# Performance work log

Hardware: AMD Instinct MI355X
Metric: run time of the kernel (lower is better)

The kernel has to match this reference:

```python
import jax, jax.numpy as jnp
import numpy as np

B, LD = 256, 64
NO, LO = 10240, 32
NM, LM = 81920, 16
EO, EM = 81920, 327680
E, HID, H, Dh, V = 128, 256, 8, 16, 10000


def masked_mean(tokens, table):
    # tokens: [N, L] int; pad id = 0
    emb = table[tokens]                            # [N, L, E]
    mask = (tokens != 0)
    s = jnp.sum(emb * mask[..., None].astype(emb.dtype), axis=1)
    lens = jnp.maximum(jnp.sum(mask, axis=1), 1).astype(emb.dtype)
    return s / lens[:, None]


def segment_softmax(scores, seg, num_segments):
    # scores: [E, ...]; softmax over entries sharing seg id (PyG softmax)
    m = jax.ops.segment_max(scores, seg, num_segments=num_segments)
    e = jnp.exp(scores - m[seg])
    s = jax.ops.segment_sum(e, seg, num_segments=num_segments)
    return e / (s[seg] + 1e-16)


def gcn_conv(x, W, b, src, dst, n):
    # PyG GCNConv: normalize=True, add_self_loops=True
    xw = x @ W
    loops = jnp.arange(n, dtype=src.dtype)
    s2 = jnp.concatenate([src, loops])
    d2 = jnp.concatenate([dst, loops])
    deg = jax.ops.segment_sum(jnp.ones_like(d2, dtype=x.dtype), d2, num_segments=n)
    dinv = deg ** -0.5  # deg >= 1 due to self loops
    norm = dinv[s2] * dinv[d2]
    out = jax.ops.segment_sum(xw[s2] * norm[:, None], d2, num_segments=n)
    return out + b


def transformer_conv(x, Wq, bq, Wk, bk, Wv, bv, Wskip, bskip, src, dst, n):
    q = (x @ Wq + bq).reshape(n, H, Dh)
    k = (x @ Wk + bk).reshape(n, H, Dh)
    v = (x @ Wv + bv).reshape(n, H, Dh)
    score = jnp.sum(q[dst] * k[src], axis=-1) / jnp.sqrt(jnp.asarray(Dh, x.dtype))  # [E, H]
    alpha = segment_softmax(score, dst, n)
    agg = jax.ops.segment_sum(alpha[:, :, None] * v[src], dst, num_segments=n)  # [n, H, Dh]
    return agg.reshape(n, H * Dh) + x @ Wskip + bskip


def global_attention(x, Wg, bg, seg, num_segments):
    gate = x @ Wg + bg                              # [N, 1]
    a = segment_softmax(gate, seg, num_segments)
    return jax.ops.segment_sum(a * x, seg, num_segments=num_segments)


def setup_inputs():
    key = jax.random.key(0)
    ks = jax.random.split(key, 20)
    sc = lambda k, shape: jax.random.normal(k, shape, dtype=jnp.float32) * 0.05
    inp = {
        "desc_tokens": jax.random.randint(ks[0], (B, LD), 0, V, dtype=jnp.int32),
        "x_tokens": jax.random.randint(ks[1], (NO, LO), 0, V, dtype=jnp.int32),
        "mini_tokens": jax.random.randint(ks[2], (NM, LM), 0, V, dtype=jnp.int32),
        "src": jax.random.randint(ks[3], (EO,), 0, NO, dtype=jnp.int32),
        "dst": jax.random.randint(ks[4], (EO,), 0, NO, dtype=jnp.int32),
        "mini_src": jax.random.randint(ks[5], (EM,), 0, NM, dtype=jnp.int32),
        "mini_dst": jax.random.randint(ks[6], (EM,), 0, NM, dtype=jnp.int32),
        "mini_batch": (jnp.arange(NM, dtype=jnp.int32) // (NM // NO)),
        "node_batch": (jnp.arange(NO, dtype=jnp.int32) // (NO // B)),
        "desc_table": sc(ks[7], (V, E)),
        "code_table": sc(ks[8], (V, E)),
        "code_table2": sc(ks[9], (V, E)),
        "Wq": sc(ks[10], (E, H * Dh)), "bq": jnp.zeros((H * Dh,), jnp.float32),
        "Wk": sc(ks[11], (E, H * Dh)), "bk": jnp.zeros((H * Dh,), jnp.float32),
        "Wv": sc(ks[12], (E, H * Dh)), "bv": jnp.zeros((H * Dh,), jnp.float32),
        "Wskip": sc(ks[13], (E, H * Dh)), "bskip": jnp.zeros((H * Dh,), jnp.float32),
        "W2": sc(ks[14], (E, HID)), "b2": jnp.zeros((HID,), jnp.float32),
        "W3": sc(ks[15], (HID, E)), "b3": jnp.zeros((E,), jnp.float32),
        "Wg": sc(ks[16], (E, 1)), "bg": jnp.zeros((1,), jnp.float32),
    }
    return inp


def reference(desc_tokens, x_tokens, mini_tokens, src, dst, mini_src, mini_dst,
              mini_batch, node_batch, desc_table, code_table, code_table2,
              Wq, bq, Wk, bk, Wv, bv, Wskip, bskip, W2, b2, W3, b3, Wg, bg):
    # encode_desc: embedding + masked mean pool -> [B, E]
    h_n = masked_mean(desc_tokens, desc_table)
    # encode_code_graph
    stmt_emb = masked_mean(x_tokens, code_table2)          # [NO, E]
    mini_emb = masked_mean(mini_tokens, code_table)        # [NM, E]
    mini_hidden = transformer_conv(mini_emb, Wq, bq, Wk, bk, Wv, bv,
                                   Wskip, bskip, mini_src, mini_dst, NM)
    mini_fn = global_attention(mini_hidden, Wg, bg, mini_batch, NO)  # [NO, E]
    mini_fn = (mini_fn + stmt_emb) * 0.5
    h = jax.nn.relu(gcn_conv(mini_fn, W2, b2, src, dst, NO))
    final_stmt = gcn_conv(h, W3, b3, src, dst, NO)
    fn_repr = global_attention(final_stmt, Wg, bg, node_batch, B)    # [B, E]
    # cosine similarity (torch eps=1e-8 clamps each norm)
    na = jnp.maximum(jnp.linalg.norm(fn_repr, axis=-1), 1e-8)
    nb = jnp.maximum(jnp.linalg.norm(h_n, axis=-1), 1e-8)
    return jnp.sum(fn_repr * h_n, axis=-1) / (na * nb)
```

## Files before the change

### kernel.cpp

```cpp
#include <hip/hip_runtime.h>
#include <hip/hip_bf16.h>
#include <math.h>

#define BB   256
#define LDE  64
#define NO   10240
#define LO   32
#define NM   81920
#define LM   16
#define EO   81920
#define EM   327680
#define ED   128
#define HIDD 256
#define NH   8
#define DH   16
#define VV   10000

static inline int nblk(long long n, int b) { return (int)((n + b - 1) / b); }

typedef __attribute__((ext_vector_type(8))) short short8;
typedef __attribute__((ext_vector_type(4))) float f32x4;

static __device__ __forceinline__ unsigned short bf16_rne(float f) {
  unsigned u = __float_as_uint(f);
  return (unsigned short)((u + 0x7fffu + ((u >> 16) & 1u)) >> 16);
}
static __device__ __forceinline__ float bf16_to_f(unsigned short h) {
  return __uint_as_float(((unsigned)h) << 16);
}
static __device__ __forceinline__ float4 b4f(ushort4 h) {
  return make_float4(bf16_to_f(h.x), bf16_to_f(h.y), bf16_to_f(h.z), bf16_to_f(h.w));
}
static __device__ __forceinline__ ushort4 f4b(float4 v) {
  return make_ushort4(bf16_rne(v.x), bf16_rne(v.y), bf16_rne(v.z), bf16_rne(v.w));
}

static __device__ __forceinline__ void gl_lds16(const void* g, void* l) {
  __builtin_amdgcn_global_load_lds(
      (const __attribute__((address_space(1))) unsigned int*)g,
      (__attribute__((address_space(3))) unsigned int*)l, 16, 0, 0);
}

struct ConvArgs {
  const float *Wq, *Wk, *Wv, *Ws, *W2, *W3;
  const float *bq, *bk, *bv, *bs;
  short8* frag;
  float* bias512;
  const float* t1; unsigned short* o1;
  const float* t2; unsigned short* o2;
  int* hist;
};
#define TBLK (2 * VV * ED / 4 / 256)
#define ZBLK ((NM + NO) / 256)
__global__ void __launch_bounds__(256)
conv_all_k(ConvArgs A) {
  int b = blockIdx.x;
  if (b < 32) {
    int g = b * 256 + threadIdx.x;
    int lane = g & 63, f = g >> 6;
    int jl = f & 7, kb = (f >> 3) & 3, ch = f >> 5;
    int cf = ch * 8 + jl;
    int c = cf * 16 + (lane & 15);
    int k0 = kb * 32 + ((lane >> 4) << 3);
    const float* wp; int cm;
    if (c < 128)      { wp = A.Wq; cm = c; }
    else if (c < 384) { int u = c - 128, t = u & 7;
                        wp = (t < 4) ? A.Wk : A.Wv; cm = (u >> 3) * 4 + (t & 3); }
    else              { wp = A.Ws; cm = c - 384; }
    short8 h;
    #pragma unroll
    for (int j = 0; j < 8; ++j)
      h[j] = (short)bf16_rne(wp[(size_t)(k0 + j) * 128 + cm]);
    A.frag[g] = h;
  } else if (b < 64) {
    int g = (b - 32) * 256 + threadIdx.x;
    const float* wp; int M, dstbase, gg;
    if (g < 4096) { wp = A.W2; M = 256; dstbase = 8192;  gg = g; }
    else          { wp = A.W3; M = 128; dstbase = 12288; gg = g - 4096; }
    int lane = gg & 63, fid = gg >> 6;
    int nt = fid % (M / 16), kb = fid / (M / 16);
    int n = nt * 16 + (lane & 15);
    int k0 = kb * 32 + ((lane >> 4) << 3);
    short8 h;
    #pragma unroll
    for (int j = 0; j < 8; ++j)
      h[j] = (short)bf16_rne(wp[(size_t)(k0 + j) * M + n]);
    A.frag[dstbase + gg] = h;
  } else if (b < 64 + TBLK) {
    int q = (b - 64) * 256 + threadIdx.x;
    const int NT = VV * ED / 4;
    if (q < NT) {
      float4 v = *(const float4*)(A.t1 + (size_t)q * 4);
      *(ushort4*)(A.o1 + (size_t)q * 4) = f4b(v);
    } else if (q < 2 * NT) {
      int q2 = q - NT;
      float4 v = *(const float4*)(A.t2 + (size_t)q2 * 4);
      *(ushort4*)(A.o2 + (size_t)q2 * 4) = f4b(v);
    }
  } else if (b < 64 + TBLK + ZBLK) {
    int i = (b - 64 - TBLK) * 256 + threadIdx.x;
    if (i < NM + NO) A.hist[i] = 0;
  } else {
    for (int c = threadIdx.x; c < 512; c += 256) {
      float v;
      if (c < 128)      v = A.bq[c];
      else if (c < 384) { int u = c - 128, t = u & 7;
                          v = (t < 4) ? A.bk[(u >> 3) * 4 + t] : A.bv[(u >> 3) * 4 + (t & 3)]; }
      else              v = A.bs[c - 384];
      A.bias512[c] = v;
    }
  }
}

template<int L>
static __device__ __forceinline__ void embed_body_f(const int* __restrict__ tokens,
                                                    const float* __restrict__ table,
                                                    float* __restrict__ out, int blk) {
  const int r = threadIdx.x >> 5, lane = threadIdx.x & 31;
  const int n0 = blk * 8;
  __shared__ int toks[8][L];
  for (int i = threadIdx.x; i < 8 * L; i += 256)
    toks[i / L][i % L] = tokens[(size_t)n0 * L + i];
  __syncthreads();
  float4 acc = make_float4(0.f, 0.f, 0.f, 0.f);
  int cnt = 0;
  #pragma unroll
  for (int l = 0; l < L; ++l) {
    int t = toks[r][l];
    float4 v = *(const float4*)(table + (size_t)t * ED + lane * 4);
    float msk = (t != 0) ? 1.f : 0.f;
    cnt += (t != 0);
    acc.x = fmaf(msk, v.x, acc.x); acc.y = fmaf(msk, v.y, acc.y);
    acc.z = fmaf(msk, v.z, acc.z); acc.w = fmaf(msk, v.w, acc.w);
  }
  float inv = 1.f / (float)(cnt > 0 ? cnt : 1);
  acc.x *= inv; acc.y *= inv; acc.z *= inv; acc.w *= inv;
  *(float4*)(out + (size_t)(n0 + r) * ED + lane * 4) = acc;
}

template<int L>
static __device__ __forceinline__ void embed_body16b(const int* __restrict__ tokens,
                                                     const unsigned short* __restrict__ table,
                                                     unsigned short* __restrict__ out, int blk) {
  const int r = threadIdx.x >> 4, lane = threadIdx.x & 15;
  const int n0 = blk * 16;
  __shared__ int toks[16][L];
  for (int i = threadIdx.x; i < 16 * L; i += 256)
    toks[i / L][i % L] = tokens[(size_t)n0 * L + i];
  __syncthreads();
  float acc[8] = {};
  int cnt = 0;
  #pragma unroll
  for (int b0 = 0; b0 < L; b0 += 16) {
    short8 vv[16];
    #pragma unroll
    for (int l = 0; l < 16; ++l) {
      int t = toks[r][b0 + l];
      vv[l] = *(const short8*)(table + (size_t)t * ED + lane * 8);
    }
    #pragma unroll
    for (int l = 0; l < 16; ++l) {
      int t = toks[r][b0 + l];
      float msk = (t != 0) ? 1.f : 0.f;
      cnt += (t != 0);
      #pragma unroll
      for (int j = 0; j < 8; ++j)
        acc[j] = fmaf(msk, bf16_to_f((unsigned short)vv[l][j]), acc[j]);
    }
  }
  float inv = 1.f / (float)(cnt > 0 ? cnt : 1);
  short8 o;
  #pragma unroll
  for (int j = 0; j < 8; ++j) o[j] = (short)bf16_rne(acc[j] * inv);
  *(short8*)(out + (size_t)(n0 + r) * ED + lane * 8) = o;
}

#define HBLK ((EM + EO) / 256)
#define MBLK (NM / 16)
#define XBLK (NO / 16)
__global__ void __launch_bounds__(256)
embed_all_k(const int* __restrict__ desc_tokens, const float* __restrict__ desc_table,
            float* __restrict__ h_n,
            const int* __restrict__ x_tokens, const unsigned short* __restrict__ ctab2,
            unsigned short* __restrict__ stmt,
            const int* __restrict__ mini_tokens, const unsigned short* __restrict__ ctab,
            unsigned short* __restrict__ miniE,
            const int* __restrict__ mini_dst, const int* __restrict__ dst,
            int* __restrict__ histm, int* __restrict__ histo) {
  int b = blockIdx.x;
  if (b < MBLK) embed_body16b<LM>(mini_tokens, ctab, miniE, b);
  else if (b < MBLK + XBLK) embed_body16b<LO>(x_tokens, ctab2, stmt, b - MBLK);
  else if (b < MBLK + XBLK + BB / 8)
    embed_body_f<LDE>(desc_tokens, desc_table, h_n, b - MBLK - XBLK);
  else {
    int e = (b - MBLK - XBLK - BB / 8) * 256 + threadIdx.x;
    if (e < EM) atomicAdd(&histm[mini_dst[e]], 1);
    else        atomicAdd(&histo[dst[e - EM]], 1);
  }
}

__global__ void scan_partials2_k(int* __restrict__ p) {
  __shared__ int sd[512];
  int base = (blockIdx.x == 0) ? 0 : NM / 256;
  int B    = (blockIdx.x == 0) ? NM / 256 : NO / 256;
  int t = threadIdx.x;
  int v = (t < B) ? p[base + t] : 0;
  sd[t] = v; __syncthreads();
  for (int off = 1; off < 512; off <<= 1) {
    int a = (t >= off) ? sd[t - off] : 0;
    __syncthreads();
    sd[t] += a;
    __syncthreads();
  }
  if (t < B) p[base + t] = sd[t] - v;
}
__global__ void scan_final2_k(const int* __restrict__ hist, const int* __restrict__ partials,
                              int* __restrict__ offsm, int* __restrict__ curm,
                              int* __restrict__ offso, int* __restrict__ curo,
                              float* __restrict__ dinv) {
  __shared__ int sd[256];
  int i = blockIdx.x * 256 + threadIdx.x;
  int v = hist[i];
  sd[threadIdx.x] = v; __syncthreads();
  for (int off = 1; off < 256; off <<= 1) {
    int a = (threadIdx.x >= off) ? sd[threadIdx.x - off] : 0;
    __syncthreads();
    sd[threadIdx.x] += a;
    __syncthreads();
  }
  int excl = sd[threadIdx.x] - v + partials[blockIdx.x];
  if (i < NM) {
    offsm[i] = excl; curm[i] = excl;
    if (i == NM - 1) offsm[NM] = excl + v;
  } else {
    int i2 = i - NM;
    offso[i2] = excl; curo[i2] = excl;
    if (i2 == NO - 1) offso[NO] = excl + v;
    dinv[i2] = 1.f / sqrtf(1.f + (float)v);
  }
}
__global__ void scatter2_k(const int* __restrict__ sm, const int* __restrict__ dm,
                           int* __restrict__ cm, int* __restrict__ km,
                           const int* __restrict__ so, const int* __restrict__ dd,
                           int* __restrict__ co, int* __restrict__ ko) {
  int e = blockIdx.x * 256 + threadIdx.x;
  if (e < EM) {
    int pos = atomicAdd(&cm[dm[e]], 1);
    km[pos] = sm[e];
  } else {
    int e2 = e - EM;
    if (e2 < EO) {
      int pos = atomicAdd(&co[dd[e2]], 1);
      ko[pos] = so[e2];
    }
  }
}

#define QKVSB (NM / 128)
#define CSUMB ((NM + NO) / 256)
__global__ void __launch_bounds__(512)
qkvs_merged_k(const unsigned short* __restrict__ Ab, const short8* __restrict__ Wf,
              const float* __restrict__ bias512, unsigned short* __restrict__ out,
              const int* __restrict__ hist, int* __restrict__ part) {
  __shared__ short8 wlds[2048];
  const int tid = threadIdx.x;
  if (blockIdx.x >= QKVSB) {
    int* sd = (int*)wlds;
    const int cb = blockIdx.x - QKVSB;
    const int i = cb * 256 + (tid & 255);
    if (tid < 256) sd[tid] = (i < NM + NO) ? hist[i] : 0;
    __syncthreads();
    for (int s = 128; s > 0; s >>= 1) {
      if (tid < s) sd[tid] += sd[tid + s];
      __syncthreads();
    }
    if (tid == 0) part[cb] = sd[0];
    return;
  }
  const int id = blockIdx.x;
  const int blk = (id & 7) * 80 + (id >> 3);
  const int n0 = blk * 128;
  const int w = tid >> 6, lane = tid & 63;
  const int r = lane & 15, qd = lane >> 4;
  const int node = n0 + w * 16 + r;
  char* myl = (char*)wlds + w * 4096;

  short8 a[4];
  #pragma unroll
  for (int kb = 0; kb < 4; ++kb)
    a[kb] = *(const short8*)(Ab + (size_t)node * ED + kb * 32 + qd * 8);

  for (int ch = 0; ch < 4; ++ch) {
    {
      const char* gs = (const char*)Wf + (size_t)ch * 32768
                     + (size_t)(w * 4) * 1024 + (size_t)lane * 16;
      char* ls = (char*)wlds + (w * 4) * 1024;
      #pragma unroll
      for (int t = 0; t < 4; ++t)
        gl_lds16(gs + t * 1024, ls + t * 1024);
    }
    __syncthreads();

    f32x4 acc[8];
    #pragma unroll
    for (int jl = 0; jl < 8; ++jl) acc[jl] = (f32x4){0.f, 0.f, 0.f, 0.f};
    #pragma unroll
    for (int kb = 0; kb < 4; ++kb)
      #pragma unroll
      for (int jl = 0; jl < 8; ++jl) {
        short8 wf = *(const short8*)((const char*)wlds
                      + ((size_t)((kb << 3) | jl) * 64 + lane) * 16);
        acc[jl] = __builtin_amdgcn_mfma_f32_16x16x32_bf16(wf, a[kb], acc[jl], 0, 0, 0);
      }
    __syncthreads();

    #pragma unroll
    for (int jl = 0; jl < 8; ++jl) {
      const int cf = ch * 8 + jl;
      const float4 bv = *(const float4*)(bias512 + cf * 16 + qd * 4);
      ushort4 o;
      o.x = bf16_rne(acc[jl][0] + bv.x);
      o.y = bf16_rne(acc[jl][1] + bv.y);
      o.z = bf16_rne(acc[jl][2] + bv.z);
      o.w = bf16_rne(acc[jl][3] + bv.w);
      *(ushort4*)(myl + r * 256 + ((jl * 32) ^ ((r & 7) << 5)) + qd * 8) = o;
    }
    #pragma unroll
    for (int t = 0; t < 4; ++t) {
      const int rr = t * 4 + qd;
      short8 v = *(const short8*)(myl + rr * 256 + (((lane & 15) * 16) ^ ((rr & 7) << 5)));
      *(short8*)(out + (size_t)(n0 + w * 16 + rr) * 512 + ch * 128 + (lane & 15) * 8) = v;
    }
    __syncthreads();
  }
}

template<bool RELU>
__global__ void __launch_bounds__(512)
mgemm_b_k(const unsigned short* __restrict__ Ab, const short8* __restrict__ Bh,
          const float* __restrict__ bias, unsigned short* __restrict__ C,
          int K, int M) {
  const int bn0 = blockIdx.x * 128;
  const int n0 = blockIdx.y * 128;
  const int tid = threadIdx.x;
  const int w = tid >> 6, lane = tid & 63;
  const int wm = (w & 3) * 2, wn = (w >> 2) * 4;
  const int r = lane & 15, qd = lane >> 4;
  const int NTm = M / 16;
  f32x4 acc[2][4];
  #pragma unroll
  for (int i = 0; i < 2; ++i)
    #pragma unroll
    for (int j = 0; j < 4; ++j) acc[i][j] = (f32x4){0.f, 0.f, 0.f, 0.f};
  const int kbn = K / 32;
  for (int kb = 0; kb < kbn; ++kb) {
    short8 bh[4];
    #pragma unroll
    for (int j = 0; j < 4; ++j)
      bh[j] = Bh[((size_t)kb * NTm + (bn0 >> 4) + wn + j) * 64 + lane];
    short8 a[2];
    #pragma unroll
    for (int i = 0; i < 2; ++i)
      a[i] = *(const short8*)(Ab + (size_t)(n0 + (wm + i) * 16 + r) * K + kb * 32 + qd * 8);
    #pragma unroll
    for (int i = 0; i < 2; ++i)
      #pragma unroll
      for (int j = 0; j < 4; ++j)
        acc[i][j] = __builtin_amdgcn_mfma_f32_16x16x32_bf16(bh[j], a[i], acc[i][j], 0, 0, 0);
  }
  #pragma unroll
  for (int i = 0; i < 2; ++i)
    #pragma unroll
    for (int j = 0; j < 4; ++j) {
      const int node = n0 + (wm + i) * 16 + r;
      const int colb = bn0 + (wn + j) * 16 + qd * 4;
      float4 bv = bias ? *(const float4*)(bias + colb) : make_float4(0.f, 0.f, 0.f, 0.f);
      float v0 = acc[i][j][0] + bv.x;
      float v1 = acc[i][j][1] + bv.y;
      float v2 = acc[i][j][2] + bv.z;
      float v3 = acc[i][j][3] + bv.w;
      if (RELU) {
        v0 = fmaxf(v0, 0.f); v1 = fmaxf(v1, 0.f);
        v2 = fmaxf(v2, 0.f); v3 = fmaxf(v3, 0.f);
      }
      ushort4 o = make_ushort4(bf16_rne(v0), bf16_rne(v1), bf16_rne(v2), bf16_rne(v3));
      *(ushort4*)(C + (size_t)node * M + colb) = o;
    }
}

__global__ void __launch_bounds__(128)
attn_fused_k(unsigned short* buf,
             const int* __restrict__ offs, const int* __restrict__ csr,
             const float* __restrict__ Wg, const float* __restrict__ bg,
             float* __restrict__ gateOut) {
  const int g = threadIdx.x >> 5, lane = threadIdx.x & 31;
  const int n = blockIdx.x * 4 + g;
  float4 q = b4f(*(const ushort4*)(buf + (size_t)n * 512 + lane * 4));
  float4 sk = b4f(*(const ushort4*)(buf + (size_t)n * 512 + 384 + lane * 4));
  float4 wg = *(const float4*)(Wg + lane * 4);
  int lo = offs[n], hi = offs[n + 1];
  float4 O = make_float4(0.f, 0.f, 0.f, 0.f);
  float m = -INFINITY, l = 0.f;
  for (int base = lo; base < hi; base += 4) {
    int rem = hi - base;
    int sidx[4];
    #pragma unroll
    for (int i = 0; i < 4; ++i) sidx[i] = (i < rem) ? csr[base + i] : 0;
    short8 kvr[4];
    #pragma unroll
    for (int i = 0; i < 4; ++i)
      kvr[i] = *(const short8*)(buf + (size_t)sidx[i] * 512 + 128 + lane * 8);
    float sc[4]; float4 vt[4];
    #pragma unroll
    for (int i = 0; i < 4; ++i) {
      float4 kt = make_float4(bf16_to_f((unsigned short)kvr[i][0]),
                              bf16_to_f((unsigned short)kvr[i][1]),
                              bf16_to_f((unsigned short)kvr[i][2]),
                              bf16_to_f((unsigned short)kvr[i][3]));
      vt[i] = make_float4(bf16_to_f((unsigned short)kvr[i][4]),
                          bf16_to_f((unsigned short)kvr[i][5]),
                          bf16_to_f((unsigned short)kvr[i][6]),
                          bf16_to_f((unsigned short)kvr[i][7]));
      float p = q.x * kt.x + q.y * kt.y + q.z * kt.z + q.w * kt.w;
      p += __shfl_xor(p, 1, 64);
      p += __shfl_xor(p, 2, 64);
      sc[i] = (i < rem) ? p * 0.25f : -INFINITY;
    }
    float mt = fmaxf(fmaxf(sc[0], sc[1]), fmaxf(sc[2], sc[3]));
    float mn = fmaxf(m, mt);
    float scale = __expf(m - mn);
    float pe[4];
    #pragma unroll
    for (int i = 0; i < 4; ++i) pe[i] = __expf(sc[i] - mn);
    l = l * scale + ((pe[0] + pe[1]) + (pe[2] + pe[3]));
    O.x = fmaf(pe[3], vt[3].x, fmaf(pe[2], vt[2].x, fmaf(pe[1], vt[1].x, fmaf(pe[0], vt[0].x, O.x * scale))));
    O.y = fmaf(pe[3], vt[3].y, fmaf(pe[2], vt[2].y, fmaf(pe[1], vt[1].y, fmaf(pe[0], vt[0].y, O.y * scale))));
    O.z = fmaf(pe[3], vt[3].z, fmaf(pe[2], vt[2].z, fmaf(pe[1], vt[1].z, fmaf(pe[0], vt[0].z, O.z * scale))));
    O.w = fmaf(pe[3], vt[3].w, fmaf(pe[2], vt[2].w, fmaf(pe[1], vt[1].w, fmaf(pe[0], vt[0].w, O.w * scale))));
    m = mn;
  }
  float inv = 1.f / (l + 1e-16f);
  float4 out = make_float4(O.x * inv + sk.x, O.y * inv + sk.y,
                           O.z * inv + sk.z, O.w * inv + sk.w);
  *(ushort4*)(buf + (size_t)n * 512 + lane * 4) = f4b(out);
  float ps = out.x * wg.x + out.y * wg.y + out.z * wg.z + out.w * wg.w;
  #pragma unroll
  for (int o = 1; o <= 16; o <<= 1) ps += __shfl_xor(ps, o, 64);
  if (lane == 0) gateOut[n] = ps + bg[0];
}

__global__ void __launch_bounds__(256)
gcn_gather_b_k(const unsigned short* __restrict__ x, const float* __restrict__ dinv,
               const int* __restrict__ offs, const int* __restrict__ csr,
               const float* __restrict__ bias, unsigned short* __restrict__ out,
               const float* __restrict__ Wg, const float* __restrict__ bg,
               float* __restrict__ gateOut) {
  const int wv = threadIdx.x >> 6, lane = threadIdx.x & 63;
  const int half = lane >> 5, cl = lane & 31;
  const int n = blockIdx.x * 4 + wv;
  float di = dinv[n];
  float4 acc = make_float4(0.f, 0.f, 0.f, 0.f);
  if (half == 0) {
    float4 xs = b4f(*(const ushort4*)(x + (size_t)n * ED + cl * 4));
    float w0 = di * di;
    acc = make_float4(w0 * xs.x, w0 * xs.y, w0 * xs.z, w0 * xs.w);
  }
  int lo = offs[n], hi = offs[n + 1];
  for (int base = lo; base < hi; base += 8) {
    int sidx[4]; bool ok[4];
    #pragma unroll
    for (int i = 0; i < 4; ++i) {
      int e = base + 2 * i + half;
      ok[i] = e < hi;
      sidx[i] = ok[i] ? csr[e] : 0;
    }
    float dw[4];
    #pragma unroll
    for (int i = 0; i < 4; ++i) dw[i] = ok[i] ? di * dinv[sidx[i]] : 0.f;
    ushort4 vr[4];
    #pragma unroll
    for (int i = 0; i < 4; ++i)
      vr[i] = *(const ushort4*)(x + (size_t)sidx[i] * ED + cl * 4);
    #pragma unroll
    for (int i = 0; i < 4; ++i) {
      float4 v = b4f(vr[i]);
      acc.x = fmaf(dw[i], v.x, acc.x); acc.y = fmaf(dw[i], v.y, acc.y);
      acc.z = fmaf(dw[i], v.z, acc.z); acc.w = fmaf(dw[i], v.w, acc.w);
    }
  }
  acc.x += __shfl_xor(acc.x, 32, 64); acc.y += __shfl_xor(acc.y, 32, 64);
  acc.z += __shfl_xor(acc.z, 32, 64); acc.w += __shfl_xor(acc.w, 32, 64);
  if (bias) {
    float4 b4 = *(const float4*)(bias + cl * 4);
    acc.x += b4.x; acc.y += b4.y; acc.z += b4.z; acc.w += b4.w;
  }
  if (half == 0)
    *(ushort4*)(out + (size_t)n * ED + cl * 4) = f4b(acc);
  if (gateOut) {
    float4 wg = *(const float4*)(Wg + cl * 4);
    float ps = acc.x * wg.x + acc.y * wg.y + acc.z * wg.z + acc.w * wg.w;
    #pragma unroll
    for (int o = 1; o <= 16; o <<= 1) ps += __shfl_xor(ps, o, 64);
    if (lane == 0) gateOut[n] = ps + bg[0];
  }
}

static __device__ __forceinline__ int lower_bound_d(const int* a, int n, int key) {
  int lo = 0, hi = n;
  while (lo < hi) { int mid = (lo + hi) >> 1; if (a[mid] < key) lo = mid + 1; else hi = mid; }
  return lo;
}
__global__ void __launch_bounds__(128)
gattn_comb_b_k(const unsigned short* __restrict__ xv, const float* __restrict__ gate,
               const int* __restrict__ seg, int Ntot,
               const unsigned short* __restrict__ other, unsigned short* __restrict__ out) {
  const int g = threadIdx.x >> 5, lane = threadIdx.x & 31;
  const int n = blockIdx.x * 4 + g;
  __shared__ int sh[4][2];
  if (lane == 0) {
    sh[g][0] = lower_bound_d(seg, Ntot, n);
    sh[g][1] = lower_bound_d(seg, Ntot, n + 1);
  }
  __syncthreads();
  int lo = sh[g][0], hi = sh[g][1];
  float m = -INFINITY;
  for (int j = lo; j < hi; ++j) m = fmaxf(m, gate[j]);
  float ssum = 0.f;
  for (int j = lo; j < hi; ++j) ssum += __expf(gate[j] - m);
  float inv = 1.f / (ssum + 1e-16f);
  float4 acc = make_float4(0.f, 0.f, 0.f, 0.f);
  for (int j = lo; j < hi; ++j) {
    float a = __expf(gate[j] - m) * inv;
    float4 v = b4f(*(const ushort4*)(xv + (size_t)j * 512 + lane * 4));
    acc.x = fmaf(a, v.x, acc.x); acc.y = fmaf(a, v.y, acc.y);
    acc.z = fmaf(a, v.z, acc.z); acc.w = fmaf(a, v.w, acc.w);
  }
  float4 o4 = b4f(*(const ushort4*)(other + (size_t)n * ED + lane * 4));
  acc.x = (acc.x + o4.x) * 0.5f; acc.y = (acc.y + o4.y) * 0.5f;
  acc.z = (acc.z + o4.z) * 0.5f; acc.w = (acc.w + o4.w) * 0.5f;
  *(ushort4*)(out + (size_t)n * ED + lane * 4) = f4b(acc);
}

__global__ void __launch_bounds__(128)
gattn_cos_k(const unsigned short* __restrict__ x, const float* __restrict__ gate,
            const int* __restrict__ seg, int Ntot,
            const float* __restrict__ hn, float* __restrict__ outp) {
  const int g = threadIdx.x >> 5, lane = threadIdx.x & 31;
  const int n = blockIdx.x * 4 + g;
  __shared__ int sh[4][2];
  if (lane == 0) {
    sh[g][0] = lower_bound_d(seg, Ntot, n);
    sh[g][1] = lower_bound_d(seg, Ntot, n + 1);
  }
  __syncthreads();
  int lo = sh[g][0], hi = sh[g][1];
  float m = -INFINITY;
  for (int j = lo; j < hi; ++j) m = fmaxf(m, gate[j]);
  float ssum = 0.f;
  for (int j = lo; j < hi; ++j) ssum += __expf(gate[j] - m);
  float inv = 1.f / (ssum + 1e-16f);
  float4 acc = make_float4(0.f, 0.f, 0.f, 0.f);
  for (int j = lo; j < hi; ++j) {
    float a = __expf(gate[j] - m) * inv;
    float4 v = b4f(*(const ushort4*)(x + (size_t)j * ED + lane * 4));
    acc.x = fmaf(a, v.x, acc.x); acc.y = fmaf(a, v.y, acc.y);
    acc.z = fmaf(a, v.z, acc.z); acc.w = fmaf(a, v.w, acc.w);
  }
  float4 hv = *(const float4*)(hn + (size_t)n * ED + lane * 4);
  float dot = acc.x * hv.x + acc.y * hv.y + acc.z * hv.z + acc.w * hv.w;
  float na  = acc.x * acc.x + acc.y * acc.y + acc.z * acc.z + acc.w * acc.w;
  float nb  = hv.x * hv.x + hv.y * hv.y + hv.z * hv.z + hv.w * hv.w;
  #pragma unroll
  for (int o = 1; o <= 16; o <<= 1) {
    dot += __shfl_xor(dot, o, 64);
    na  += __shfl_xor(na,  o, 64);
    nb  += __shfl_xor(nb,  o, 64);
  }
  if (lane == 0)
    outp[n] = dot / (fmaxf(sqrtf(na), 1e-8f) * fmaxf(sqrtf(nb), 1e-8f));
}

constexpr size_t OFF_HN    = 0;
constexpr size_t OFF_STMT  = OFF_HN    + (size_t)BB * ED;
constexpr size_t OFF_A     = OFF_STMT  + (size_t)NO * ED;
constexpr size_t OFF_CT    = OFF_A     + (size_t)NM * ED;
constexpr size_t OFF_QKVS  = OFF_CT    + (size_t)VV * ED;
constexpr size_t T0        = OFF_QKVS  + (size_t)NM * 256;
constexpr size_t OFF_GATE  = T0;
constexpr size_t OFF_GATE2 = OFF_GATE  + (size_t)NM;
constexpr size_t OFF_DINV  = OFF_GATE2 + (size_t)NO;
constexpr size_t OFF_HISTM = OFF_DINV  + (size_t)NO;
constexpr size_t OFF_HISTO = OFF_HISTM + (size_t)NM;
constexpr size_t OFF_OFFSM = OFF_HISTO + (size_t)NO;
constexpr size_t OFF_CURM  = OFF_OFFSM + (size_t)NM + 1;
constexpr size_t OFF_CSRM  = OFF_CURM  + (size_t)NM;
constexpr size_t OFF_OFFSO = OFF_CSRM  + (size_t)EM;
constexpr size_t OFF_CURO  = OFF_OFFSO + (size_t)NO + 1;
constexpr size_t OFF_CSRO  = OFF_CURO  + (size_t)NO;
constexpr size_t OFF_PART  = OFF_CSRO  + (size_t)EO;
constexpr size_t OFF_B512  = OFF_PART  + 512;
constexpr size_t OFF_WFHI  = OFF_B512  + 512;
constexpr size_t OFF_MFN   = OFF_A;
constexpr size_t OFF_AGG   = OFF_MFN   + (size_t)NO * ED;
constexpr size_t OFF_H     = OFF_AGG   + (size_t)NO * ED;
constexpr size_t OFF_T     = OFF_H     + (size_t)NO * HIDD;
constexpr size_t OFF_FIN   = OFF_T     + (size_t)NO * ED;

extern "C" void kernel_launch(void* const* d_in, const int* in_sizes, int n_in,
                              void* d_out, int out_size, void* d_ws, size_t ws_size,
                              hipStream_t stream) {
  const int* desc_tokens = (const int*)d_in[0];
  const int* x_tokens    = (const int*)d_in[1];
  const int* mini_tokens = (const int*)d_in[2];
  const int* src         = (const int*)d_in[3];
  const int* dst         = (const int*)d_in[4];
  const int* mini_src    = (const int*)d_in[5];
  const int* mini_dst    = (const int*)d_in[6];
  const int* mini_batch  = (const int*)d_in[7];
  const int* node_batch  = (const int*)d_in[8];
  const float* desc_table  = (const float*)d_in[9];
  const float* code_table  = (const float*)d_in[10];
  const float* code_table2 = (const float*)d_in[11];
  const float* Wq = (const float*)d_in[12]; const float* bq = (const float*)d_in[13];
  const float* Wk = (const float*)d_in[14]; const float* bk = (const float*)d_in[15];
  const float* Wv = (const float*)d_in[16]; const float* bv = (const float*)d_in[17];
  const float* Wskip = (const float*)d_in[18]; const float* bskip = (const float*)d_in[19];
  const float* W2 = (const float*)d_in[20]; const float* b2 = (const float*)d_in[21];
  const float* W3 = (const float*)d_in[22]; const float* b3 = (const float*)d_in[23];
  const float* Wg = (const float*)d_in[24]; const float* bg = (const float*)d_in[25];

  float* ws = (float*)d_ws;
  float* h_n   = ws + OFF_HN;
  unsigned short* stmt_b  = (unsigned short*)(ws + OFF_STMT);
  unsigned short* miniE_b = (unsigned short*)(ws + OFF_A);
  unsigned short* ctab_b  = (unsigned short*)(ws + OFF_CT);
  unsigned short* ctab2_b = ctab_b + (size_t)VV * ED;
  unsigned short* qkvs_b  = (unsigned short*)(ws + OFF_QKVS);
  float* gate  = ws + OFF_GATE;
  float* gate2 = ws + OFF_GATE2;
  float* dinv  = ws + OFF_DINV;
  int* histm = (int*)(ws + OFF_HISTM);
  int* histo = (int*)(ws + OFF_HISTO);
  int* offsm = (int*)(ws + OFF_OFFSM);
  int* curm  = (int*)(ws + OFF_CURM);
  int* csrm  = (int*)(ws + OFF_CSRM);
  int* offso = (int*)(ws + OFF_OFFSO);
  int* curo  = (int*)(ws + OFF_CURO);
  int* csro  = (int*)(ws + OFF_CSRO);
  int* part  = (int*)(ws + OFF_PART);
  float* bias512 = ws + OFF_B512;
  short8* wfrag = (short8*)(ws + OFF_WFHI);
  unsigned short* mini_fn_b = (unsigned short*)(ws + OFF_MFN);
  unsigned short* aggb_b    = (unsigned short*)(ws + OFF_AGG);
  unsigned short* hbuf_b    = (unsigned short*)(ws + OFF_H);
  unsigned short* tbuf_b    = (unsigned short*)(ws + OFF_T);
  unsigned short* finalS_b  = (unsigned short*)(ws + OFF_FIN);
  float* outp    = (float*)d_out;

  ConvArgs ca;
  ca.Wq = Wq; ca.Wk = Wk; ca.Wv = Wv; ca.Ws = Wskip; ca.W2 = W2; ca.W3 = W3;
  ca.bq = bq; ca.bk = bk; ca.bv = bv; ca.bs = bskip;
  ca.frag = wfrag; ca.bias512 = bias512;
  ca.t1 = code_table;  ca.o1 = ctab_b;
  ca.t2 = code_table2; ca.o2 = ctab2_b;
  ca.hist = histm;
  conv_all_k<<<64 + TBLK + ZBLK + 1, 256, 0, stream>>>(ca);

  embed_all_k<<<MBLK + XBLK + BB / 8 + HBLK, 256, 0, stream>>>(
      desc_tokens, desc_table, h_n, x_tokens, ctab2_b, stmt_b,
      mini_tokens, ctab_b, miniE_b, mini_dst, dst, histm, histo);

  qkvs_merged_k<<<QKVSB + CSUMB, 512, 0, stream>>>(miniE_b, wfrag, bias512, qkvs_b,
                                                   histm, part);

  scan_partials2_k<<<2, 512, 0, stream>>>(part);
  scan_final2_k<<<(NM + NO) / 256, 256, 0, stream>>>(histm, part, offsm, curm,
                                                     offso, curo, dinv);
  scatter2_k<<<nblk(EM + EO, 256), 256, 0, stream>>>(mini_src, mini_dst, curm, csrm,
                                                     src, dst, curo, csro);

  attn_fused_k<<<NM / 4, 128, 0, stream>>>(qkvs_b, offsm, csrm, Wg, bg, gate);

  gattn_comb_b_k<<<NO / 4, 128, 0, stream>>>(qkvs_b, gate, mini_batch, NM,
                                             stmt_b, mini_fn_b);

  gcn_gather_b_k<<<NO / 4, 256, 0, stream>>>(mini_fn_b, dinv, offso, csro, nullptr,
                                             aggb_b, nullptr, nullptr, nullptr);
  { dim3 g(HIDD / 128, NO / 128);
    mgemm_b_k<true><<<g, 512, 0, stream>>>(aggb_b, wfrag + 8192, b2, hbuf_b, ED, HIDD); }

  { dim3 g(1, NO / 128);
    mgemm_b_k<false><<<g, 512, 0, stream>>>(hbuf_b, wfrag + 12288, nullptr, tbuf_b, HIDD, ED); }
  gcn_gather_b_k<<<NO / 4, 256, 0, stream>>>(tbuf_b, dinv, offso, csro, b3, finalS_b,
                                             Wg, bg, gate2);

  gattn_cos_k<<<BB / 4, 128, 0, stream>>>(finalS_b, gate2, node_batch, NO, h_n, outp);
}
```

Before: 327.6 us.

## Fuse mini-token embedding pooling into the QKVS GEMM kernel via LDS

The masked-mean embedding of mini tokens is now computed inside the QKVS GEMM blocks. Each block pools its 128 rows straight into a swizzled LDS tile and loads the A fragments from there, so the bf16 miniE intermediate is never written to or read back from global memory. The x-token embed path also drops its batched 16-load prefetch for a simple per-token loop. In exchange the GEMM blocks take on gather latency and an extra 8 KB of LDS for tokens, which may reduce occupancy or overlap.

```diff
diff --git a/kernel.cpp b/kernel.cpp
--- a/kernel.cpp
+++ b/kernel.cpp
@@ -139,9 +139,9 @@
 }
 
 template<int L>
-static __device__ __forceinline__ void embed_body16b(const int* __restrict__ tokens,
-                                                     const unsigned short* __restrict__ table,
-                                                     unsigned short* __restrict__ out, int blk) {
+static __device__ __forceinline__ void embed_body16(const int* __restrict__ tokens,
+                                                    const unsigned short* __restrict__ table,
+                                                    unsigned short* __restrict__ out, int blk) {
   const int r = threadIdx.x >> 4, lane = threadIdx.x & 15;
   const int n0 = blk * 16;
   __shared__ int toks[16][L];
@@ -151,22 +151,14 @@
   float acc[8] = {};
   int cnt = 0;
   #pragma unroll
-  for (int b0 = 0; b0 < L; b0 += 16) {
-    short8 vv[16];
-    #pragma unroll
-    for (int l = 0; l < 16; ++l) {
-      int t = toks[r][b0 + l];
-      vv[l] = *(const short8*)(table + (size_t)t * ED + lane * 8);
-    }
-    #pragma unroll
-    for (int l = 0; l < 16; ++l) {
-      int t = toks[r][b0 + l];
-      float msk = (t != 0) ? 1.f : 0.f;
-      cnt += (t != 0);
-      #pragma unroll
-      for (int j = 0; j < 8; ++j)
-        acc[j] = fmaf(msk, bf16_to_f((unsigned short)vv[l][j]), acc[j]);
-    }
+  for (int l = 0; l < L; ++l) {
+    int t = toks[r][l];
+    short8 v = *(const short8*)(table + (size_t)t * ED + lane * 8);
+    float msk = (t != 0) ? 1.f : 0.f;
+    cnt += (t != 0);
+    #pragma unroll
+    for (int j = 0; j < 8; ++j)
+      acc[j] = fmaf(msk, bf16_to_f((unsigned short)v[j]), acc[j]);
   }
   float inv = 1.f / (float)(cnt > 0 ? cnt : 1);
   short8 o;
@@ -176,24 +168,20 @@
 }
 
 #define HBLK ((EM + EO) / 256)
-#define MBLK (NM / 16)
 #define XBLK (NO / 16)
 __global__ void __launch_bounds__(256)
 embed_all_k(const int* __restrict__ desc_tokens, const float* __restrict__ desc_table,
             float* __restrict__ h_n,
             const int* __restrict__ x_tokens, const unsigned short* __restrict__ ctab2,
             unsigned short* __restrict__ stmt,
-            const int* __restrict__ mini_tokens, const unsigned short* __restrict__ ctab,
-            unsigned short* __restrict__ miniE,
             const int* __restrict__ mini_dst, const int* __restrict__ dst,
             int* __restrict__ histm, int* __restrict__ histo) {
   int b = blockIdx.x;
-  if (b < MBLK) embed_body16b<LM>(mini_tokens, ctab, miniE, b);
-  else if (b < MBLK + XBLK) embed_body16b<LO>(x_tokens, ctab2, stmt, b - MBLK);
-  else if (b < MBLK + XBLK + BB / 8)
-    embed_body_f<LDE>(desc_tokens, desc_table, h_n, b - MBLK - XBLK);
+  if (b < XBLK) embed_body16<LO>(x_tokens, ctab2, stmt, b);
+  else if (b < XBLK + BB / 8)
+    embed_body_f<LDE>(desc_tokens, desc_table, h_n, b - XBLK);
   else {
-    int e = (b - MBLK - XBLK - BB / 8) * 256 + threadIdx.x;
+    int e = (b - XBLK - BB / 8) * 256 + threadIdx.x;
     if (e < EM) atomicAdd(&histm[mini_dst[e]], 1);
     else        atomicAdd(&histo[dst[e - EM]], 1);
   }
@@ -259,10 +247,12 @@
 #define QKVSB (NM / 128)
 #define CSUMB ((NM + NO) / 256)
 __global__ void __launch_bounds__(512)
-qkvs_merged_k(const unsigned short* __restrict__ Ab, const short8* __restrict__ Wf,
-              const float* __restrict__ bias512, unsigned short* __restrict__ out,
+qkvs_merged_k(const int* __restrict__ mini_tokens, const unsigned short* __restrict__ ctab,
+              const short8* __restrict__ Wf, const float* __restrict__ bias512,
+              unsigned short* __restrict__ out,
               const int* __restrict__ hist, int* __restrict__ part) {
   __shared__ short8 wlds[2048];
+  __shared__ int toks[128][16];
   const int tid = threadIdx.x;
   if (blockIdx.x >= QKVSB) {
     int* sd = (int*)wlds;
@@ -280,16 +270,48 @@
   const int id = blockIdx.x;
   const int blk = (id & 7) * 80 + (id >> 3);
   const int n0 = blk * 128;
+
+  for (int i = tid; i < 128 * 16; i += 512)
+    ((int*)toks)[i] = mini_tokens[(size_t)n0 * 16 + i];
+  __syncthreads();
+
+  char* alds = (char*)wlds;
+  #pragma unroll
+  for (int t = 0; t < 4; ++t) {
+    const int task = t * 512 + tid;
+    const int row = task >> 4, ch = task & 15;
+    float acc[8] = {};
+    int cnt = 0;
+    #pragma unroll
+    for (int l = 0; l < 16; ++l) {
+      int tok = toks[row][l];
+      short8 v = *(const short8*)(ctab + (size_t)tok * ED + ch * 8);
+      float msk = (tok != 0) ? 1.f : 0.f;
+      cnt += (tok != 0);
+      #pragma unroll
+      for (int j = 0; j < 8; ++j)
+        acc[j] = fmaf(msk, bf16_to_f((unsigned short)v[j]), acc[j]);
+    }
+    float inv = 1.f / (float)(cnt > 0 ? cnt : 1);
+    short8 o;
+    #pragma unroll
+    for (int j = 0; j < 8; ++j) o[j] = (short)bf16_rne(acc[j] * inv);
+    *(short8*)(alds + ((row * 256 + ch * 16) ^ ((row & 7) << 4))) = o;
+  }
+  __syncthreads();
+
   const int w = tid >> 6, lane = tid & 63;
   const int r = lane & 15, qd = lane >> 4;
-  const int node = n0 + w * 16 + r;
+  const int lrow = w * 16 + r;
+  short8 a[4];
+  #pragma unroll
+  for (int kb = 0; kb < 4; ++kb) {
+    const int ch = kb * 4 + qd;
+    a[kb] = *(const short8*)(alds + ((lrow * 256 + ch * 16) ^ ((lrow & 7) << 4)));
+  }
+  __syncthreads();
+
   char* myl = (char*)wlds + w * 4096;
-
-  short8 a[4];
-  #pragma unroll
-  for (int kb = 0; kb < 4; ++kb)
-    a[kb] = *(const short8*)(Ab + (size_t)node * ED + kb * 32 + qd * 8);
-
   for (int ch = 0; ch < 4; ++ch) {
     {
       const char* gs = (const char*)Wf + (size_t)ch * 32768
@@ -632,7 +654,6 @@
   float* ws = (float*)d_ws;
   float* h_n   = ws + OFF_HN;
   unsigned short* stmt_b  = (unsigned short*)(ws + OFF_STMT);
-  unsigned short* miniE_b = (unsigned short*)(ws + OFF_A);
   unsigned short* ctab_b  = (unsigned short*)(ws + OFF_CT);
   unsigned short* ctab2_b = ctab_b + (size_t)VV * ED;
   unsigned short* qkvs_b  = (unsigned short*)(ws + OFF_QKVS);
@@ -666,12 +687,12 @@
   ca.hist = histm;
   conv_all_k<<<64 + TBLK + ZBLK + 1, 256, 0, stream>>>(ca);
 
-  embed_all_k<<<MBLK + XBLK + BB / 8 + HBLK, 256, 0, stream>>>(
+  embed_all_k<<<XBLK + BB / 8 + HBLK, 256, 0, stream>>>(
       desc_tokens, desc_table, h_n, x_tokens, ctab2_b, stmt_b,
-      mini_tokens, ctab_b, miniE_b, mini_dst, dst, histm, histo);
-
-  qkvs_merged_k<<<QKVSB + CSUMB, 512, 0, stream>>>(miniE_b, wfrag, bias512, qkvs_b,
-                                                   histm, part);
+      mini_dst, dst, histm, histo);
+
+  qkvs_merged_k<<<QKVSB + CSUMB, 512, 0, stream>>>(mini_tokens, ctab_b, wfrag,
+                                                   bias512, qkvs_b, histm, part);
 
   scan_partials2_k<<<2, 512, 0, stream>>>(part);
   scan_final2_k<<<(NM + NO) / 256, 256, 0, stream>>>(histm, part, offsm, curm,
```

After: 337.9 us. 1.03x slower.
